# Performance work log

Measured on AMD Instinct MI355X. Metric: run time of the kernel, lower is better.

The kernel has to match this reference:

```python
import jax, jax.numpy as jnp
import numpy as np

B, S, D = 1, 2048, 2048
H, KV, HD = 32, 8, 64
POWER = 100000.0


def _rotary(x):
    # x: [B, h, S, HD]; faithful to RotaryEncoder: freqs = pos / div_term
    rot_dim = HD // 2
    pos = jnp.arange(S, dtype=x.dtype)
    div = POWER ** (jnp.arange(0, HD, 2, dtype=x.dtype) / HD)  # [HD//2]
    freqs = pos[:, None] / div  # [S, HD//2]
    cos, sin = jnp.cos(freqs), jnp.sin(freqs)
    x_rot, x_pass = x[..., :rot_dim], x[..., rot_dim:]
    h = rot_dim // 2
    rot_half = jnp.concatenate([-x_rot[..., h:], x_rot[..., :h]], axis=-1)
    return jnp.concatenate([x_rot * cos + rot_half * sin, x_pass], axis=-1)


def setup_inputs() -> dict:
    key = jax.random.key(0)
    k1, k2, k3 = jax.random.split(key, 3)
    hidden_states = jax.random.normal(k1, (B, S, D), dtype=jnp.float32)
    op_size = H * HD + 2 * KV * HD
    Wqkv = jax.random.normal(k2, (D, op_size), dtype=jnp.float32) * 0.02
    Wo = jax.random.normal(k3, (H * HD, D), dtype=jnp.float32) * 0.02
    causal = jnp.tril(jnp.ones((S, S), dtype=bool))
    attention_mask = jnp.where(causal, 0.0, -1e9).astype(jnp.float32)[None, None]
    return {"hidden_states": hidden_states, "attention_mask": attention_mask,
            "Wqkv": Wqkv, "Wo": Wo}


def reference(hidden_states, attention_mask, Wqkv, Wo):
    groups = H // KV
    qkv = hidden_states @ Wqkv  # [B, S, op_size]
    qpos = H * HD
    q = qkv[..., :qpos].reshape(B, S, H, HD).transpose(0, 2, 1, 3)
    k = qkv[..., qpos:qpos + KV * HD].reshape(B, S, KV, HD).transpose(0, 2, 1, 3)
    v = qkv[..., qpos + KV * HD:].reshape(B, S, KV, HD).transpose(0, 2, 1, 3)
    q = _rotary(q)
    k = _rotary(k)
    k = jnp.repeat(k, groups, axis=1)  # GQA repeat_interleave -> [B, H, S, HD]
    v = jnp.repeat(v, groups, axis=1)
    scores = jnp.einsum('bhqd,bhkd->bhqk', q, k) / jnp.sqrt(jnp.float32(HD))
    scores = scores + attention_mask[..., :S]
    attn = jax.nn.softmax(scores.astype(jnp.float32), axis=-1).astype(v.dtype)
    out = jnp.einsum('bhqk,bhkd->bhqd', attn, v)
    out = out.transpose(0, 2, 1, 3).reshape(B, S, H * HD)
    return out @ Wo
```

## Files before the change

### kernel.cpp

```cpp
#include <hip/hip_runtime.h>
#include <hip/hip_bf16.h>
#include <cstdint>
#include <cstddef>

#define S_LEN 2048
#define D_MODEL 2048
#define NH 32
#define NKV 8
#define HDIM 64
#define OPSZ 3072
#define KOFF 2048
#define VOFF 2560

typedef float    floatx4 __attribute__((ext_vector_type(4)));
typedef __bf16   bf16x8  __attribute__((ext_vector_type(8)));
typedef __bf16   bf16x4  __attribute__((ext_vector_type(4)));
typedef __bf16   bf16_t;
typedef _Float16 f16_t;
typedef _Float16 f16x4   __attribute__((ext_vector_type(4)));
typedef _Float16 f16x8   __attribute__((ext_vector_type(8)));

__device__ __forceinline__ void gld16(const void* g, void* l) {
  __builtin_amdgcn_global_load_lds((__attribute__((address_space(1))) void*)(void*)g,
                                   (__attribute__((address_space(3))) void*)l,
                                   16, 0, 0);
}

__global__ __launch_bounds__(256)
void prep_kernel(const float* __restrict__ X, const float* __restrict__ Wqkv,
                 const float* __restrict__ Wo, bf16_t* __restrict__ Xb,
                 bf16_t* __restrict__ WqkvT, bf16_t* __restrict__ WoT) {
  const int bx = blockIdx.x;
  const int k0 = blockIdx.y * 32;
  const int tx = threadIdx.x & 31, ty = threadIdx.x >> 5;
  if (bx < 160) {
    __shared__ float tile[32][33];
    const float* W; bf16_t* Wt; int N, n0;
    if (bx < 96) { W = Wqkv; Wt = WqkvT; N = OPSZ;    n0 = bx * 32; }
    else         { W = Wo;   Wt = WoT;   N = D_MODEL; n0 = (bx - 96) * 32; }
#pragma unroll
    for (int i = 0; i < 32; i += 8)
      tile[ty + i][tx] = W[(size_t)(k0 + ty + i) * N + n0 + tx];
    __syncthreads();
#pragma unroll
    for (int i = 0; i < 32; i += 8)
      Wt[(size_t)(n0 + ty + i) * D_MODEL + k0 + tx] = (bf16_t)tile[tx][ty + i];
  } else {
    const int n0 = (bx - 160) * 32;
#pragma unroll
    for (int i = 0; i < 32; i += 8) {
      const size_t idx = (size_t)(k0 + ty + i) * D_MODEL + n0 + tx;
      Xb[idx] = (bf16_t)X[idx];
    }
  }
}

#define GEMM64_CORE(A_, Bt_, K_, m0_, n0_)                                        \
  const int tid = threadIdx.x;                                                    \
  const int wave = tid >> 6;                                                      \
  const int lane = tid & 63;                                                      \
  const int lane15 = lane & 15;                                                   \
  const int quad = lane >> 4;                                                     \
  const int wm = (wave & 1) * 32;                                                 \
  const int wn = (wave >> 1) * 64;                                                \
  floatx4 acc[2][4];                                                              \
  _Pragma("unroll") for (int i = 0; i < 2; i++)                                   \
    _Pragma("unroll") for (int j = 0; j < 4; j++)                                 \
      acc[i][j] = floatx4{0.f, 0.f, 0.f, 0.f};                                    \
  {                                                                               \
                                                  \
    const int ca0 = tid, ca1 = tid + 256;                                         \
    const int apan0 = ca0 >> 8, ar0 = (ca0 & 255) >> 2, ac0 = (ca0 & 3) * 8;      \
    const int apan1 = ca1 >> 8, ar1 = (ca1 & 255) >> 2, ac1 = (ca1 & 3) * 8;      \
                  \
    int bpan[4], br[4], bc[4];                                                    \
    _Pragma("unroll") for (int i = 0; i < 4; i++) {                               \
      const int c = tid + i * 256;                                                \
      bpan[i] = c >> 9; br[i] = (c & 511) >> 2; bc[i] = (c & 3) * 8;              \
    }                                                                             \
    bf16_t* lA0 = &As[(wave * 64) * 8];                                           \
    bf16_t* lA1 = &As[(256 + wave * 64) * 8];                                     \
    for (int k0 = 0; k0 < (K_); k0 += 64) {                                       \
      __syncthreads();                                                            \
      gld16((A_) + (size_t)((m0_) + ar0) * (K_) + k0 + apan0 * 32 + ac0, lA0);    \
      gld16((A_) + (size_t)((m0_) + ar1) * (K_) + k0 + apan1 * 32 + ac1, lA1);    \
      _Pragma("unroll") for (int i = 0; i < 4; i++)                               \
        gld16((Bt_) + (size_t)((n0_) + br[i]) * (K_) + k0 + bpan[i] * 32 + bc[i], \
              &Bs[(i * 256 + wave * 64) * 8]);                                    \
      __syncthreads();                                                            \
      _Pragma("unroll") for (int kt = 0; kt < 2; kt++) {                          \
        bf16x8 af[2], bfr[4];                                                     \
        _Pragma("unroll") for (int mi = 0; mi < 2; mi++)                          \
          af[mi] = *(const bf16x8*)&As[kt * 2048 + (wm + mi * 16 + lane15) * 32 + quad * 8]; \
        _Pragma("unroll") for (int ni = 0; ni < 4; ni++)                          \
          bfr[ni] = *(const bf16x8*)&Bs[kt * 4096 + (wn + ni * 16 + lane15) * 32 + quad * 8]; \
        _Pragma("unroll") for (int mi = 0; mi < 2; mi++)                          \
          _Pragma("unroll") for (int ni = 0; ni < 4; ni++)                        \
            acc[mi][ni] = __builtin_amdgcn_mfma_f32_16x16x32_bf16(af[mi], bfr[ni],\
                                                                  acc[mi][ni], 0, 0, 0); \
      }                                                                           \
    }                                                                             \
  }

#define QSCALE 0.18033688011112042f
__global__ __launch_bounds__(256, 3)
void gemm_qkv_rope(const bf16_t* __restrict__ A, const bf16_t* __restrict__ Bt,
                   bf16_t* __restrict__ Qr, bf16_t* __restrict__ Kr,
                   f16_t* __restrict__ VtG) {
  __shared__ bf16_t As[2 * 64 * 32];
  __shared__ bf16_t Bs[2 * 128 * 32];
  const int m0 = blockIdx.y * 64;
  const int n0 = blockIdx.x * 128;
  GEMM64_CORE(A, Bt, D_MODEL, m0, n0)

  const int colbase = n0 + wn;
  const int s0 = m0 + wm;

  if (colbase < VOFF) {
    const bool isQ = (colbase < KOFF);
    const float k2 = 0.51905126483f;
    const float pj0 = exp2f(-(float)lane15 * k2);
    const float pj1 = pj0 * 0.0031622776601684f;
    bf16_t* dst = isQ ? (Qr + ((size_t)(colbase >> 6) * S_LEN) * HDIM)
                      : (Kr + ((size_t)((colbase - KOFF) >> 6) * S_LEN) * HDIM);
    const float qs = isQ ? QSCALE : 1.0f;
#pragma unroll
    for (int mi = 0; mi < 2; mi++) {
#pragma unroll
      for (int r = 0; r < 4; r++) {
        const int s = s0 + mi * 16 + quad * 4 + r;
        const float sf = (float)s;
        float s0s, s0c, s1s, s1c;
        __sincosf(sf * pj0, &s0s, &s0c);
        __sincosf(sf * pj1, &s1s, &s1c);
        const float x0 = acc[mi][0][r], x1 = acc[mi][1][r];
        bf16_t* row = dst + (size_t)s * HDIM + lane15;
        row[0]  = (bf16_t)((x0 * s0c - x1 * s0s) * qs);
        row[16] = (bf16_t)((x1 * s1c + x0 * s1s) * qs);
        row[32] = (bf16_t)(acc[mi][2][r] * qs);
        row[48] = (bf16_t)(acc[mi][3][r] * qs);
      }
    }
  } else {
    const int kvv = (colbase - VOFF) >> 6;
    f16_t* dst = VtG + (size_t)kvv * HDIM * S_LEN;
#pragma unroll
    for (int mi = 0; mi < 2; mi++) {
      const int s = s0 + mi * 16 + quad * 4;
#pragma unroll
      for (int ni = 0; ni < 4; ni++) {
        const int d = ni * 16 + lane15;
        f16x4 tv;
#pragma unroll
        for (int r = 0; r < 4; r++) tv[r] = (f16_t)acc[mi][ni][r];
        *(f16x4*)&dst[(size_t)d * S_LEN + s] = tv;
      }
    }
  }
}

__global__ __launch_bounds__(256, 3)
void gemm_bt_f32out(const bf16_t* __restrict__ A, const bf16_t* __restrict__ Bt,
                    float* __restrict__ C, int M, int N, int K) {
  __shared__ bf16_t As[2 * 64 * 32];
  __shared__ bf16_t Bs[2 * 128 * 32];
  const int m0 = blockIdx.y * 64;
  const int n0 = blockIdx.x * 128;
  GEMM64_CORE(A, Bt, K, m0, n0)

#pragma unroll
  for (int mi = 0; mi < 2; mi++)
#pragma unroll
    for (int r = 0; r < 4; r++) {
      const int row = m0 + wm + mi * 16 + quad * 4 + r;
#pragma unroll
      for (int ni = 0; ni < 4; ni++) {
        const int col = n0 + wn + ni * 16 + lane15;
        C[(size_t)row * N + col] = acc[mi][ni][r];
      }
    }
}

#define KST 72
#define VST 136
__global__ __launch_bounds__(256, 4)
void flash_kernel(const bf16_t* __restrict__ Qr, const bf16_t* __restrict__ Kr,
                  const f16_t* __restrict__ VtG, bf16_t* __restrict__ attn) {
  __shared__ bf16_t Ks[128 * KST];
  __shared__ f16_t  Vt[64 * VST];

  const int tid = threadIdx.x;
  const int wave = tid >> 6;
  const int lane = tid & 63;
  const int lane15 = lane & 15;
  const int quad = lane >> 4;
  const int bx = blockIdx.x;
  const int h = bx & 31;
  const int qblk = 31 - (bx >> 5);
  const int q0 = qblk * 64;
  const int rq = q0 + wave * 16;
  const int kv = h >> 2;
  const size_t kbase = (size_t)kv * S_LEN * HDIM;
  const size_t vbase = (size_t)kv * HDIM * S_LEN;

  const int kr_ = tid >> 3, kc_ = (tid & 7) * 8;
  const int vd_ = tid >> 4, vc_ = (tid & 15) * 8;

  bf16x8 aq[2];
#pragma unroll
  for (int kt = 0; kt < 2; kt++)
    aq[kt] = *(const bf16x8*)&Qr[((size_t)h * S_LEN + rq + lane15) * HDIM + kt * 32 + quad * 8];

  float m_run = -1e30f, l_run = 0.f;
  floatx4 o[4];
#pragma unroll
  for (int dt = 0; dt < 4; dt++) o[dt] = floatx4{0.f, 0.f, 0.f, 0.f};

  const int nk = (qblk + 2) >> 1;

  for (int t = 0; t < nk; ++t) {
    const int p0 = t * 128;
    __syncthreads();
#pragma unroll
    for (int i = 0; i < 4; i++) {
      const int r = kr_ + i * 32;
      *(bf16x8*)&Ks[r * KST + kc_] = *(const bf16x8*)&Kr[kbase + (size_t)(p0 + r) * HDIM + kc_];
    }
#pragma unroll
    for (int i = 0; i < 4; i++) {
      const int d = vd_ + i * 16;
      *(f16x8*)&Vt[d * VST + vc_] = *(const f16x8*)&VtG[vbase + (size_t)d * S_LEN + p0 + vc_];
    }
    __syncthreads();

    floatx4 sc[8];
#pragma unroll
    for (int nt = 0; nt < 8; nt++) sc[nt] = floatx4{0.f, 0.f, 0.f, 0.f};
#pragma unroll
    for (int kt = 0; kt < 2; kt++) {
#pragma unroll
      for (int nt = 0; nt < 8; nt++) {
        const bf16x8 ak = *(const bf16x8*)&Ks[(nt * 16 + lane15) * KST + kt * 32 + quad * 8];
        sc[nt] = __builtin_amdgcn_mfma_f32_16x16x32_bf16(ak, aq[kt], sc[nt], 0, 0, 0);
      }
    }

    if (p0 + 127 > rq) {
#pragma unroll
      for (int nt = 0; nt < 8; nt++)
#pragma unroll
        for (int r = 0; r < 4; r++) {
          const int kpos = p0 + nt * 16 + quad * 4 + r;
          const int qrow = rq + lane15;
          if (kpos > qrow) sc[nt][r] = -1e30f;
        }
    }

    float mt = fmaxf(fmaxf(sc[0][0], sc[0][1]), fmaxf(sc[0][2], sc[0][3]));
#pragma unroll
    for (int nt = 1; nt < 8; nt++)
#pragma unroll
      for (int r = 0; r < 4; r++) mt = fmaxf(mt, sc[nt][r]);
    mt = fmaxf(mt, __shfl_xor(mt, 16));
    mt = fmaxf(mt, __shfl_xor(mt, 32));
    const float mnew = fmaxf(m_run, mt);
    const float alpha = exp2f(m_run - mnew);
    m_run = mnew;
    float rs = 0.f;
    f16x4 ph[8];
#pragma unroll
    for (int nt = 0; nt < 8; nt++) {
      f16x4 pv;
#pragma unroll
      for (int r = 0; r < 4; r++) {
        const float p = exp2f(sc[nt][r] - mnew);
        rs += p;
        pv[r] = (f16_t)p;
      }
      ph[nt] = pv;
    }
    rs += __shfl_xor(rs, 16);
    rs += __shfl_xor(rs, 32);
    l_run = l_run * alpha + rs;
#pragma unroll
    for (int dt = 0; dt < 4; dt++)
#pragma unroll
      for (int r = 0; r < 4; r++) o[dt][r] *= alpha;

#pragma unroll
    for (int kt4 = 0; kt4 < 8; kt4++) {
#pragma unroll
      for (int dt = 0; dt < 4; dt++) {
        const f16x4 av = *(const f16x4*)&Vt[(dt * 16 + lane15) * VST + kt4 * 16 + quad * 4];
        o[dt] = __builtin_amdgcn_mfma_f32_16x16x16f16(av, ph[kt4], o[dt], 0, 0, 0);
      }
    }
  }

  const float inv = 1.0f / l_run;
  const int s = rq + lane15;
#pragma unroll
  for (int dt = 0; dt < 4; dt++) {
    bf16x4 tv;
#pragma unroll
    for (int r = 0; r < 4; r++) tv[r] = (bf16_t)(o[dt][r] * inv);
    *(bf16x4*)&attn[(size_t)s * D_MODEL + h * HDIM + dt * 16 + quad * 4] = tv;
  }
}

extern "C" void kernel_launch(void* const* d_in, const int* in_sizes, int n_in,
                              void* d_out, int out_size, void* d_ws, size_t ws_size,
                              hipStream_t stream) {
  (void)in_sizes; (void)n_in; (void)out_size; (void)ws_size;
  const float* hidden = (const float*)d_in[0];
  const float* Wqkv = (const float*)d_in[2];
  const float* Wo   = (const float*)d_in[3];
  float* out = (float*)d_out;

  char* ws = (char*)d_ws;
  size_t off = 0;
  auto alloc = [&](size_t bytes) -> void* {
    void* p = ws + off;
    off += (bytes + 255) & ~(size_t)255;
    return p;
  };
  bf16_t* Xb    = (bf16_t*)alloc((size_t)S_LEN * D_MODEL * 2);
  bf16_t* WqkvT = (bf16_t*)alloc((size_t)OPSZ * D_MODEL * 2);
  bf16_t* WoT   = (bf16_t*)alloc((size_t)D_MODEL * D_MODEL * 2);
  bf16_t* Qr    = (bf16_t*)alloc((size_t)NH * S_LEN * HDIM * 2);
  bf16_t* Kr    = (bf16_t*)alloc((size_t)NKV * S_LEN * HDIM * 2);
  f16_t*  VtG   = (f16_t*) alloc((size_t)NKV * HDIM * S_LEN * 2);
  bf16_t* attn  = (bf16_t*)alloc((size_t)S_LEN * D_MODEL * 2);

  prep_kernel<<<dim3(224, 64), 256, 0, stream>>>(hidden, Wqkv, Wo, Xb, WqkvT, WoT);
  gemm_qkv_rope<<<dim3(OPSZ / 128, S_LEN / 64), 256, 0, stream>>>(Xb, WqkvT, Qr, Kr, VtG);
  flash_kernel<<<dim3(32 * NH), 256, 0, stream>>>(Qr, Kr, VtG, attn);
  gemm_bt_f32out<<<dim3(D_MODEL / 128, S_LEN / 64), 256, 0, stream>>>(attn, WoT, out, S_LEN, D_MODEL, D_MODEL);
}
```

Baseline: 219.9 us.

## Load flash K/V tiles via global_load_lds with XOR-swizzled LDS layout

Replaces register-staged K and V tile copies in the flash attention kernel with direct global-to-LDS loads, using an XOR swizzle instead of padded strides to avoid bank conflicts. The causal mask check is hoisted so only the last tile runs the masking code. The max and sum reductions are also restructured into trees to shorten dependency chains. This removes VGPR round-trips for tile loads but adds swizzle address math and relies on the gld16 per-lane layout matching the swizzle.

After: 229.0 us. +4.1%, slower.

```diff
diff --git a/kernel.cpp b/kernel.cpp
--- a/kernel.cpp
+++ b/kernel.cpp
@@ -68,11 +68,9 @@
     _Pragma("unroll") for (int j = 0; j < 4; j++)                                 \
       acc[i][j] = floatx4{0.f, 0.f, 0.f, 0.f};                                    \
   {                                                                               \
-                                                  \
     const int ca0 = tid, ca1 = tid + 256;                                         \
     const int apan0 = ca0 >> 8, ar0 = (ca0 & 255) >> 2, ac0 = (ca0 & 3) * 8;      \
     const int apan1 = ca1 >> 8, ar1 = (ca1 & 255) >> 2, ac1 = (ca1 & 3) * 8;      \
-                  \
     int bpan[4], br[4], bc[4];                                                    \
     _Pragma("unroll") for (int i = 0; i < 4; i++) {                               \
       const int c = tid + i * 256;                                                \
@@ -181,13 +179,11 @@
     }
 }
 
-#define KST 72
-#define VST 136
 __global__ __launch_bounds__(256, 4)
 void flash_kernel(const bf16_t* __restrict__ Qr, const bf16_t* __restrict__ Kr,
                   const f16_t* __restrict__ VtG, bf16_t* __restrict__ attn) {
-  __shared__ bf16_t Ks[128 * KST];
-  __shared__ f16_t  Vt[64 * VST];
+  __shared__ bf16_t Ks[128 * 64];
+  __shared__ f16_t  Vt[64 * 128];
 
   const int tid = threadIdx.x;
   const int wave = tid >> 6;
@@ -203,8 +199,24 @@
   const size_t kbase = (size_t)kv * S_LEN * HDIM;
   const size_t vbase = (size_t)kv * HDIM * S_LEN;
 
-  const int kr_ = tid >> 3, kc_ = (tid & 7) * 8;
-  const int vd_ = tid >> 4, vc_ = (tid & 15) * 8;
+  int krow[4], kcol[4], vrow[4], vcol[4];
+#pragma unroll
+  for (int i = 0; i < 4; i++) {
+    const int c = tid + i * 256;
+    krow[i] = c >> 3;
+    kcol[i] = ((c & 7) ^ (krow[i] & 7)) * 8;
+    vrow[i] = c >> 4;
+    vcol[i] = ((c & 15) ^ (vrow[i] & 15)) * 8;
+  }
+
+  int akoff[2];
+#pragma unroll
+  for (int kt = 0; kt < 2; kt++)
+    akoff[kt] = (((kt * 4 + quad) ^ (lane15 & 7)) * 8);
+  int avoff[8];
+#pragma unroll
+  for (int kt4 = 0; kt4 < 8; kt4++)
+    avoff[kt4] = (((kt4 * 2 + (quad >> 1)) ^ lane15) * 8) + (quad & 1) * 4;
 
   bf16x8 aq[2];
 #pragma unroll
@@ -218,19 +230,14 @@
 
   const int nk = (qblk + 2) >> 1;
 
-  for (int t = 0; t < nk; ++t) {
-    const int p0 = t * 128;
+  auto process_tile = [&](int p0, bool masked) {
     __syncthreads();
 #pragma unroll
-    for (int i = 0; i < 4; i++) {
-      const int r = kr_ + i * 32;
-      *(bf16x8*)&Ks[r * KST + kc_] = *(const bf16x8*)&Kr[kbase + (size_t)(p0 + r) * HDIM + kc_];
-    }
-#pragma unroll
-    for (int i = 0; i < 4; i++) {
-      const int d = vd_ + i * 16;
-      *(f16x8*)&Vt[d * VST + vc_] = *(const f16x8*)&VtG[vbase + (size_t)d * S_LEN + p0 + vc_];
-    }
+    for (int i = 0; i < 4; i++)
+      gld16(Kr + kbase + (size_t)(p0 + krow[i]) * HDIM + kcol[i], &Ks[(tid + i * 256) * 8]);
+#pragma unroll
+    for (int i = 0; i < 4; i++)
+      gld16(VtG + vbase + (size_t)vrow[i] * S_LEN + p0 + vcol[i], &Vt[(tid + i * 256) * 8]);
     __syncthreads();
 
     floatx4 sc[8];
@@ -240,45 +247,50 @@
     for (int kt = 0; kt < 2; kt++) {
 #pragma unroll
       for (int nt = 0; nt < 8; nt++) {
-        const bf16x8 ak = *(const bf16x8*)&Ks[(nt * 16 + lane15) * KST + kt * 32 + quad * 8];
+        const bf16x8 ak = *(const bf16x8*)&Ks[(nt * 16 + lane15) * 64 + akoff[kt]];
         sc[nt] = __builtin_amdgcn_mfma_f32_16x16x32_bf16(ak, aq[kt], sc[nt], 0, 0, 0);
       }
     }
 
-    if (p0 + 127 > rq) {
+    if (masked) {
 #pragma unroll
       for (int nt = 0; nt < 8; nt++)
 #pragma unroll
         for (int r = 0; r < 4; r++) {
           const int kpos = p0 + nt * 16 + quad * 4 + r;
-          const int qrow = rq + lane15;
-          if (kpos > qrow) sc[nt][r] = -1e30f;
+          if (kpos > rq + lane15) sc[nt][r] = -1e30f;
         }
     }
 
-    float mt = fmaxf(fmaxf(sc[0][0], sc[0][1]), fmaxf(sc[0][2], sc[0][3]));
-#pragma unroll
-    for (int nt = 1; nt < 8; nt++)
-#pragma unroll
-      for (int r = 0; r < 4; r++) mt = fmaxf(mt, sc[nt][r]);
+    float tm[8];
+#pragma unroll
+    for (int nt = 0; nt < 8; nt++)
+      tm[nt] = fmaxf(fmaxf(sc[nt][0], sc[nt][1]), fmaxf(sc[nt][2], sc[nt][3]));
+    tm[0] = fmaxf(tm[0], tm[1]); tm[2] = fmaxf(tm[2], tm[3]);
+    tm[4] = fmaxf(tm[4], tm[5]); tm[6] = fmaxf(tm[6], tm[7]);
+    tm[0] = fmaxf(tm[0], tm[2]); tm[4] = fmaxf(tm[4], tm[6]);
+    float mt = fmaxf(tm[0], tm[4]);
     mt = fmaxf(mt, __shfl_xor(mt, 16));
     mt = fmaxf(mt, __shfl_xor(mt, 32));
     const float mnew = fmaxf(m_run, mt);
     const float alpha = exp2f(m_run - mnew);
     m_run = mnew;
-    float rs = 0.f;
+
     f16x4 ph[8];
+    float rsv[8];
 #pragma unroll
     for (int nt = 0; nt < 8; nt++) {
-      f16x4 pv;
-#pragma unroll
-      for (int r = 0; r < 4; r++) {
-        const float p = exp2f(sc[nt][r] - mnew);
-        rs += p;
-        pv[r] = (f16_t)p;
-      }
+      float p0e = exp2f(sc[nt][0] - mnew);
+      float p1e = exp2f(sc[nt][1] - mnew);
+      float p2e = exp2f(sc[nt][2] - mnew);
+      float p3e = exp2f(sc[nt][3] - mnew);
+      rsv[nt] = (p0e + p1e) + (p2e + p3e);
+      f16x4 pv; pv[0] = (f16_t)p0e; pv[1] = (f16_t)p1e; pv[2] = (f16_t)p2e; pv[3] = (f16_t)p3e;
       ph[nt] = pv;
     }
+    rsv[0] += rsv[1]; rsv[2] += rsv[3]; rsv[4] += rsv[5]; rsv[6] += rsv[7];
+    rsv[0] += rsv[2]; rsv[4] += rsv[6];
+    float rs = rsv[0] + rsv[4];
     rs += __shfl_xor(rs, 16);
     rs += __shfl_xor(rs, 32);
     l_run = l_run * alpha + rs;
@@ -291,11 +303,14 @@
     for (int kt4 = 0; kt4 < 8; kt4++) {
 #pragma unroll
       for (int dt = 0; dt < 4; dt++) {
-        const f16x4 av = *(const f16x4*)&Vt[(dt * 16 + lane15) * VST + kt4 * 16 + quad * 4];
+        const f16x4 av = *(const f16x4*)&Vt[(dt * 16 + lane15) * 128 + avoff[kt4]];
         o[dt] = __builtin_amdgcn_mfma_f32_16x16x16f16(av, ph[kt4], o[dt], 0, 0, 0);
       }
     }
-  }
+  };
+
+  for (int t = 0; t < nk - 1; ++t) process_tile(t * 128, false);
+  process_tile((nk - 1) * 128, true);
 
   const float inv = 1.0f / l_run;
   const int s = rq + lane15;
```
